# Performance work log

Hardware: AMD Instinct MI355X
Metric: run time of the kernel (lower is better)

## Reference

```python
import jax, jax.numpy as jnp
import numpy as np

NUM_WIRES = 20
DEPTH = 4


def setup_inputs() -> dict:
    key = jax.random.key(0)
    x = jax.random.normal(key, (NUM_WIRES,), dtype=jnp.float32)
    return {"x": x}


def _apply_1q(state, gate, wire):
    # state: flat [2^n] complex; apply 2x2 gate on `wire`
    s = state.reshape(2 ** wire, 2, -1)
    return jnp.einsum('ab,ibj->iaj', gate, s).reshape(-1)


def _apply_cnot(state, control):
    # CNOT on adjacent wires (control, control+1): flip target where control==1
    s = state.reshape(2 ** control, 2, 2, -1)
    s = jnp.concatenate([s[:, :1], s[:, 1:, ::-1]], axis=1)
    return s.reshape(-1)


def _simulate(x):
    n = NUM_WIRES
    state = jnp.zeros(2 ** n, dtype=jnp.complex64).at[0].set(1.0)
    half = (x.astype(jnp.float32) * 0.5)
    c = jnp.cos(half).astype(jnp.complex64)  # [n]
    s = jnp.sin(half).astype(jnp.complex64)  # [n]
    for _ in range(DEPTH):
        for w in range(n):
            cw, sw = c[w], s[w]
            rx = jnp.stack([jnp.stack([cw, -1j * sw]), jnp.stack([-1j * sw, cw])])
            ry = jnp.stack([jnp.stack([cw, -sw]), jnp.stack([sw, cw])])
            state = _apply_1q(state, rx, w)
            state = _apply_1q(state, ry, w)
        for w in range(n - 1):
            state = _apply_cnot(state, w)
    probs = jnp.abs(state) ** 2  # real float32 [2^n]
    expz = []
    for i in range(n):
        p = probs.reshape(2 ** i, 2, -1).sum(axis=(0, 2))
        expz.append(p[0] - p[1])
    return jnp.stack(expz).astype(jnp.float32)  # [n] <Z_i>


def reference(x):
    return _simulate(x)
```

## Files before the change

### kernel.cpp

```cpp
#include <hip/hip_runtime.h>


#define NW 20

__device__ __forceinline__ float2 cmul(float2 a, float2 b) {
    return make_float2(a.x*b.x - a.y*b.y, a.x*b.y + a.y*b.x);
}

__device__ __forceinline__ void apply_gate(float2& a0, float2& a1,
                                           float2 u00, float2 u01,
                                           float2 u10, float2 u11) {
    float2 b0, b1;
    b0.x = u00.x*a0.x - u00.y*a0.y + u01.x*a1.x - u01.y*a1.y;
    b0.y = u00.x*a0.y + u00.y*a0.x + u01.x*a1.y + u01.y*a1.x;
    b1.x = u10.x*a0.x - u10.y*a0.y + u11.x*a1.x - u11.y*a1.y;
    b1.y = u10.x*a0.y + u10.y*a0.x + u11.x*a1.y + u11.y*a1.x;
    a0 = b0; a1 = b1;
}

__device__ __forceinline__ unsigned swz(unsigned l) { return l ^ ((l >> 3) & 14u); }

__global__ void prep_gates(const float* __restrict__ x, float2* __restrict__ G) {
    int w = threadIdx.x;
    if (w < NW) {
        float h = 0.5f * x[w];
        float c = cosf(h), s = sinf(h);
        float cc = c*c, ss = s*s, cs = c*s;
        G[w*4+0] = make_float2(cc,  ss);
        G[w*4+1] = make_float2(-cs, -cs);
        G[w*4+2] = make_float2(cs,  -cs);
        G[w*4+3] = make_float2(cc,  -ss);
    }
}

template<int MODE>
__global__ __launch_bounds__(1024) void stageA(const float2* __restrict__ src,
                                               float2* __restrict__ dst,
                                               const float2* __restrict__ G) {
    __shared__ float4 ldsv[2048];
    float2* lds = (float2*)ldsv;
    unsigned t   = threadIdx.x;
    unsigned H   = blockIdx.x;
    unsigned Hp  = H ^ (H >> 1);
    unsigned inj = (H & 1u) << 11;
    unsigned l   = t * 4u;
    unsigned gl  = (l ^ (l >> 1)) ^ inj;

    float2 a0, a1, a2, a3;
    if (MODE == 1) {
        const float4* qp = (const float4*)(src + ((size_t)Hp << 12) + (gl & ~3u));
        float4 q0 = qp[0], q1 = qp[1];
        float2 e0 = make_float2(q0.x, q0.y), e1 = make_float2(q0.z, q0.w);
        float2 e2 = make_float2(q1.x, q1.y), e3 = make_float2(q1.z, q1.w);
        bool s1 = (gl & 1u) != 0u, s2 = (gl & 2u) != 0u;
        float2 f0 = s1 ? e1 : e0, f1 = s1 ? e0 : e1;
        float2 f2 = s1 ? e3 : e2, f3 = s1 ? e2 : e3;
        float2 g0 = s2 ? f2 : f0, g1 = s2 ? f3 : f1;
        float2 g2 = s2 ? f0 : f2, g3 = s2 ? f1 : f3;
        a0 = g0; a1 = g1; a2 = g3; a3 = g2;
    } else {
        float2 P = make_float2(1.0f, 0.0f);
        #pragma unroll
        for (int b = 12; b <= 19; b++)
            P = cmul(P, G[(19-b)*4 + (int)((Hp >> (b-12)) & 1u)*2]);
        #pragma unroll
        for (int b = 2; b <= 11; b++)
            P = cmul(P, G[(19-b)*4 + (int)((gl >> b) & 1u)*2]);
        float2 aa[4];
        #pragma unroll
        for (int k = 0; k < 4; k++) {
            unsigned mm = (gl ^ (unsigned)(k ^ (k >> 1))) & 3u;
            float2 f = cmul(G[19*4 + (int)(mm & 1u)*2], G[18*4 + (int)((mm >> 1) & 1u)*2]);
            aa[k] = cmul(P, f);
        }
        a0 = aa[0]; a1 = aa[1]; a2 = aa[2]; a3 = aa[3];
    }

    {
        float2 u00 = G[76], u01 = G[77], u10 = G[78], u11 = G[79];
        apply_gate(a0, a1, u00, u01, u10, u11);
        apply_gate(a2, a3, u00, u01, u10, u11);
    }
    {
        float2 u00 = G[72], u01 = G[73], u10 = G[74], u11 = G[75];
        apply_gate(a0, a2, u00, u01, u10, u11);
        apply_gate(a1, a3, u00, u01, u10, u11);
    }
    lds[swz(l+0u)] = a0; lds[swz(l+1u)] = a1;
    lds[swz(l+2u)] = a2; lds[swz(l+3u)] = a3;
    __syncthreads();

    #pragma unroll
    for (int p = 2; p <= 11; p++) {
        int w = 19 - p;
        float2 u00 = G[w*4], u01 = G[w*4+1], u10 = G[w*4+2], u11 = G[w*4+3];
        unsigned mask = (1u << p) - 1u;
        #pragma unroll
        for (int i = 0; i < 2; i++) {
            unsigned kk = (unsigned)i*1024u + t;
            unsigned l0 = ((kk & ~mask) << 1) | (kk & mask);
            unsigned l1 = l0 | (1u << p);
            unsigned s0 = swz(l0), s1i = swz(l1);
            float2 b0 = lds[s0], b1 = lds[s1i];
            apply_gate(b0, b1, u00, u01, u10, u11);
            if (p < 11) { lds[s0] = b0; lds[s1i] = b1; }
            else {
                dst[((size_t)H << 12) + l0] = b0;
                dst[((size_t)H << 12) + l1] = b1;
            }
        }
        if (p < 11) __syncthreads();
    }
}

template<int FUSE>
__global__ __launch_bounds__(1024) void stageB(float2* __restrict__ st,
                                               const float2* __restrict__ G,
                                               float* __restrict__ partial) {
    __shared__ float4 ldsv[2048];
    float2* lds = (float2*)ldsv;
    unsigned t  = threadIdx.x;
    unsigned bb = blockIdx.x;
    unsigned m  = t & 15u, hk = t >> 4;
    unsigned h0 = hk << 1;
    unsigned hsA = h0, hsB = h0 | 1u, hsC = h0 | 128u, hsD = h0 | 129u;
    size_t base = ((size_t)bb << 4) | m;
    float2 a0 = st[((size_t)hsA << 12) | base];
    float2 a1 = st[((size_t)hsB << 12) | base];
    float2 a2 = st[((size_t)hsC << 12) | base];
    float2 a3 = st[((size_t)hsD << 12) | base];

    {
        float2 u00 = G[28], u01 = G[29], u10 = G[30], u11 = G[31];
        apply_gate(a0, a1, u00, u01, u10, u11);
        apply_gate(a2, a3, u00, u01, u10, u11);
    }
    {
        float2 u00 = G[0], u01 = G[1], u10 = G[2], u11 = G[3];
        apply_gate(a0, a2, u00, u01, u10, u11);
        apply_gate(a1, a3, u00, u01, u10, u11);
    }
    lds[(hsA << 4) | m] = a0; lds[(hsB << 4) | m] = a1;
    lds[(hsC << 4) | m] = a2; lds[(hsD << 4) | m] = a3;
    __syncthreads();

    #pragma unroll
    for (int q = 1; q <= 5; q++) {
        int w = 7 - q;
        float2 u00 = G[w*4], u01 = G[w*4+1], u10 = G[w*4+2], u11 = G[w*4+3];
        unsigned mq = (1u << q) - 1u;
        #pragma unroll
        for (int i = 0; i < 2; i++) {
            unsigned kk = (unsigned)i*1024u + t;
            unsigned mm = kk & 15u, hh = kk >> 4;
            unsigned hA = ((hh & ~mq) << 1) | (hh & mq);
            unsigned ci0 = (hA << 4) | mm, ci1 = ci0 | (1u << (4 + q));
            float2 b0 = lds[ci0], b1 = lds[ci1];
            apply_gate(b0, b1, u00, u01, u10, u11);
            lds[ci0] = b0; lds[ci1] = b1;
        }
        __syncthreads();
    }

    float acc[NW];
    if (FUSE) {
        #pragma unroll
        for (int w = 0; w < NW; w++) acc[w] = 0.0f;
    }
    {
        float2 u00 = G[4], u01 = G[5], u10 = G[6], u11 = G[7];
        #pragma unroll
        for (int i = 0; i < 2; i++) {
            unsigned kk = (unsigned)i*1024u + t;
            unsigned mm = kk & 15u, hh = kk >> 4;
            unsigned hA = ((hh & ~63u) << 1) | (hh & 63u);
            unsigned ci0 = (hA << 4) | mm, ci1 = ci0 | (1u << 10);
            float2 b0 = lds[ci0], b1 = lds[ci1];
            apply_gate(b0, b1, u00, u01, u10, u11);
            if (!FUSE) {
                st[((size_t)(ci0 >> 4) << 12) | ((size_t)bb << 4) | mm] = b0;
                st[((size_t)(ci1 >> 4) << 12) | ((size_t)bb << 4) | mm] = b1;
            } else {
                #pragma unroll
                for (int e = 0; e < 2; e++) {
                    unsigned ci = e ? ci1 : ci0;
                    float2 bv  = e ? b1 : b0;
                    unsigned Y = ((ci >> 4) << 12) | (bb << 4) | mm;
                    unsigned y = Y;
                    y ^= y >> 1; y ^= y >> 2; y ^= y >> 4; y ^= y >> 8; y ^= y >> 16;
                    float p = bv.x*bv.x + bv.y*bv.y;
                    #pragma unroll
                    for (int w = 0; w < NW; w++) {
                        unsigned bit = (y >> (19 - w)) & 1u;
                        acc[w] += __uint_as_float(__float_as_uint(p) | (bit << 31));
                    }
                }
            }
        }
    }

    if (FUSE) {
        __syncthreads();
        float* redf = (float*)ldsv;
        #pragma unroll
        for (int w = 0; w < NW; w++) {
            float v = acc[w];
            #pragma unroll
            for (int off = 32; off; off >>= 1) v += __shfl_down(v, off, 64);
            if ((t & 63u) == 0u) redf[(t >> 6)*NW + w] = v;
        }
        __syncthreads();
        if (t < NW) {
            float s = 0.0f;
            #pragma unroll
            for (int wv = 0; wv < 16; wv++) s += redf[wv*NW + (int)t];
            partial[bb*NW + t] = s;
        }
    }
}

__global__ __launch_bounds__(256) void reduce_out(const float* __restrict__ partial,
                                                  float* __restrict__ out) {
    __shared__ float red[4*NW];
    unsigned t = threadIdx.x;
    float vals[NW];
    #pragma unroll
    for (int w = 0; w < NW; w++) vals[w] = partial[t*NW + w];
    #pragma unroll
    for (int w = 0; w < NW; w++) {
        float v = vals[w];
        #pragma unroll
        for (int off = 32; off; off >>= 1) v += __shfl_down(v, off, 64);
        if ((t & 63u) == 0u) red[(t >> 6)*NW + w] = v;
    }
    __syncthreads();
    if (t < NW) out[t] = red[t] + red[NW+t] + red[2*NW+t] + red[3*NW+t];
}

extern "C" void kernel_launch(void* const* d_in, const int* in_sizes, int n_in,
                              void* d_out, int out_size, void* d_ws, size_t ws_size,
                              hipStream_t stream) {
    (void)in_sizes; (void)n_in; (void)out_size; (void)ws_size;
    const float* x = (const float*)d_in[0];
    float* out = (float*)d_out;

    char* ws = (char*)d_ws;
    float2* gates   = (float2*)ws;
    float*  partial = (float*)(ws + 1024);
    float2* buf0    = (float2*)(ws + 65536);
    float2* buf1    = (float2*)(ws + 65536 + (size_t)(8u << 20));

    prep_gates<<<1, 32, 0, stream>>>(x, gates);
    stageA<0><<<256, 1024, 0, stream>>>(buf1 , buf0, gates);
    stageB<0><<<256, 1024, 0, stream>>>(buf0, gates, nullptr);
    stageA<1><<<256, 1024, 0, stream>>>(buf0, buf1, gates);
    stageB<0><<<256, 1024, 0, stream>>>(buf1, gates, nullptr);
    stageA<1><<<256, 1024, 0, stream>>>(buf1, buf0, gates);
    stageB<1><<<256, 1024, 0, stream>>>(buf0, gates, partial);
    reduce_out<<<1, 256, 0, stream>>>(partial, out);
}
```

Measured before the change: 77.15 us.

## Keep eight amplitudes per thread and apply gates via registers and lane shuffles

Both stage kernels now hold eight amplitudes per thread in registers. Gates on register bits are applied directly, bit positions are exchanged across lanes with xor-shuffles, and only a single shared-memory transpose with one barrier remains, instead of ten barriered LDS passes. Blocks shrink to 512 threads. The fused final stage also derives most Z expectations from a single parity-signed difference instead of accumulating per element. This trades LDS traffic and synchronisation for more register pressure and shuffle instructions.

Measured after the change: 72.75 us. -5.7%, faster.

```diff
diff --git a/kernel.cpp b/kernel.cpp
--- a/kernel.cpp
+++ b/kernel.cpp
@@ -18,7 +18,36 @@
     a0 = b0; a1 = b1;
 }
 
-__device__ __forceinline__ unsigned swz(unsigned l) { return l ^ ((l >> 3) & 14u); }
+__device__ __forceinline__ float2 shflx(float2 v, int m) {
+    float2 r;
+    r.x = __shfl_xor(v.x, m, 64);
+    r.y = __shfl_xor(v.y, m, 64);
+    return r;
+}
+
+template<int A>
+__device__ __forceinline__ void gate_regbit(float2 (&amp)[8], const float2* __restrict__ Gw) {
+    float2 u00 = Gw[0], u01 = Gw[1], u10 = Gw[2], u11 = Gw[3];
+    #pragma unroll
+    for (int r = 0; r < 8; r++)
+        if (!(r & (1 << A)))
+            apply_gate(amp[r], amp[r | (1 << A)], u00, u01, u10, u11);
+}
+
+template<int A, int LM>
+__device__ __forceinline__ void swap_reg_lane(float2 (&amp)[8], unsigned lane) {
+    bool hb = (lane & (unsigned)LM) != 0u;
+    #pragma unroll
+    for (int r = 0; r < 8; r++) {
+        if (!(r & (1 << A))) {
+            float2 lo = amp[r], hi = amp[r | (1 << A)];
+            float2 xs = hb ? lo : hi;
+            float2 ys = shflx(xs, LM);
+            amp[r]            = hb ? ys : lo;
+            amp[r | (1 << A)] = hb ? hi : ys;
+        }
+    }
+}
 
 __global__ void prep_gates(const float* __restrict__ x, float2* __restrict__ G) {
     int w = threadIdx.x;
@@ -34,186 +63,155 @@
 }
 
 template<int MODE>
-__global__ __launch_bounds__(1024) void stageA(const float2* __restrict__ src,
-                                               float2* __restrict__ dst,
-                                               const float2* __restrict__ G) {
-    __shared__ float4 ldsv[2048];
-    float2* lds = (float2*)ldsv;
-    unsigned t   = threadIdx.x;
-    unsigned H   = blockIdx.x;
-    unsigned Hp  = H ^ (H >> 1);
-    unsigned inj = (H & 1u) << 11;
-    unsigned l   = t * 4u;
-    unsigned gl  = (l ^ (l >> 1)) ^ inj;
-
-    float2 a0, a1, a2, a3;
+__global__ __launch_bounds__(512) void stageA(const float2* __restrict__ src,
+                                              float2* __restrict__ dst,
+                                              const float2* __restrict__ G) {
+    __shared__ float2 lds[4096];
+    const unsigned t = threadIdx.x;
+    const unsigned lane = t & 63u, wv = t >> 6;
+    const unsigned H   = blockIdx.x;
+    const unsigned Hp  = H ^ (H >> 1);
+    const unsigned inj = (H & 1u) << 11;
+    const unsigned lb  = (wv << 9) | (lane << 3);
+    const unsigned gb  = (lb ^ (lb >> 1)) ^ inj;
+
+    float2 amp[8];
     if (MODE == 1) {
-        const float4* qp = (const float4*)(src + ((size_t)Hp << 12) + (gl & ~3u));
-        float4 q0 = qp[0], q1 = qp[1];
-        float2 e0 = make_float2(q0.x, q0.y), e1 = make_float2(q0.z, q0.w);
-        float2 e2 = make_float2(q1.x, q1.y), e3 = make_float2(q1.z, q1.w);
-        bool s1 = (gl & 1u) != 0u, s2 = (gl & 2u) != 0u;
-        float2 f0 = s1 ? e1 : e0, f1 = s1 ? e0 : e1;
-        float2 f2 = s1 ? e3 : e2, f3 = s1 ? e2 : e3;
-        float2 g0 = s2 ? f2 : f0, g1 = s2 ? f3 : f1;
-        float2 g2 = s2 ? f0 : f2, g3 = s2 ? f1 : f3;
-        a0 = g0; a1 = g1; a2 = g3; a3 = g2;
+        const float4* q = (const float4*)(src + ((size_t)Hp << 12) + (gb & ~7u));
+        float4 q0 = q[0], q1 = q[1], q2 = q[2], q3 = q[3];
+        float2 e0 = make_float2(q0.x,q0.y), e1 = make_float2(q0.z,q0.w);
+        float2 e2 = make_float2(q1.x,q1.y), e3 = make_float2(q1.z,q1.w);
+        float2 e4 = make_float2(q2.x,q2.y), e5 = make_float2(q2.z,q2.w);
+        float2 e6 = make_float2(q3.x,q3.y), e7 = make_float2(q3.z,q3.w);
+        bool f = (gb & 4u) != 0u;
+        amp[0] = f ? e4 : e0;  amp[1] = f ? e5 : e1;
+        amp[2] = f ? e7 : e3;  amp[3] = f ? e6 : e2;
+        amp[4] = f ? e2 : e6;  amp[5] = f ? e3 : e7;
+        amp[6] = f ? e1 : e5;  amp[7] = f ? e0 : e4;
     } else {
         float2 P = make_float2(1.0f, 0.0f);
         #pragma unroll
         for (int b = 12; b <= 19; b++)
             P = cmul(P, G[(19-b)*4 + (int)((Hp >> (b-12)) & 1u)*2]);
         #pragma unroll
-        for (int b = 2; b <= 11; b++)
-            P = cmul(P, G[(19-b)*4 + (int)((gl >> b) & 1u)*2]);
-        float2 aa[4];
-        #pragma unroll
-        for (int k = 0; k < 4; k++) {
-            unsigned mm = (gl ^ (unsigned)(k ^ (k >> 1))) & 3u;
-            float2 f = cmul(G[19*4 + (int)(mm & 1u)*2], G[18*4 + (int)((mm >> 1) & 1u)*2]);
-            aa[k] = cmul(P, f);
-        }
-        a0 = aa[0]; a1 = aa[1]; a2 = aa[2]; a3 = aa[3];
-    }
-
-    {
-        float2 u00 = G[76], u01 = G[77], u10 = G[78], u11 = G[79];
-        apply_gate(a0, a1, u00, u01, u10, u11);
-        apply_gate(a2, a3, u00, u01, u10, u11);
-    }
-    {
-        float2 u00 = G[72], u01 = G[73], u10 = G[74], u11 = G[75];
-        apply_gate(a0, a2, u00, u01, u10, u11);
-        apply_gate(a1, a3, u00, u01, u10, u11);
-    }
-    lds[swz(l+0u)] = a0; lds[swz(l+1u)] = a1;
-    lds[swz(l+2u)] = a2; lds[swz(l+3u)] = a3;
+        for (int b = 3; b <= 11; b++)
+            P = cmul(P, G[(19-b)*4 + (int)((gb >> b) & 1u)*2]);
+        float2 Tt[8];
+        #pragma unroll
+        for (int j = 0; j < 8; j++) {
+            float2 v = cmul(G[18*4 + ((j>>1)&1)*2], G[19*4 + (j&1)*2]);
+            v = cmul(G[17*4 + ((j>>2)&1)*2], v);
+            Tt[j] = cmul(P, v);
+        }
+        bool f = (gb & 4u) != 0u;
+        amp[0] = f ? Tt[4] : Tt[0];  amp[1] = f ? Tt[5] : Tt[1];
+        amp[2] = f ? Tt[7] : Tt[3];  amp[3] = f ? Tt[6] : Tt[2];
+        amp[4] = f ? Tt[2] : Tt[6];  amp[5] = f ? Tt[3] : Tt[7];
+        amp[6] = f ? Tt[1] : Tt[5];  amp[7] = f ? Tt[0] : Tt[4];
+    }
+
+    gate_regbit<0>(amp, G + 19*4);
+    gate_regbit<1>(amp, G + 18*4);
+    gate_regbit<2>(amp, G + 17*4);
+    swap_reg_lane<0,1>(amp, lane);
+    swap_reg_lane<1,2>(amp, lane);
+    swap_reg_lane<2,4>(amp, lane);
+    gate_regbit<0>(amp, G + 16*4);
+    gate_regbit<1>(amp, G + 15*4);
+    gate_regbit<2>(amp, G + 14*4);
+    swap_reg_lane<0,8>(amp, lane);
+    swap_reg_lane<1,16>(amp, lane);
+    swap_reg_lane<2,32>(amp, lane);
+    gate_regbit<0>(amp, G + 13*4);
+    gate_regbit<1>(amp, G + 12*4);
+    gate_regbit<2>(amp, G + 11*4);
+    #pragma unroll
+    for (int k = 0; k < 8; k++) lds[(wv << 9) | ((unsigned)k << 6) | lane] = amp[k];
     __syncthreads();
-
-    #pragma unroll
-    for (int p = 2; p <= 11; p++) {
-        int w = 19 - p;
-        float2 u00 = G[w*4], u01 = G[w*4+1], u10 = G[w*4+2], u11 = G[w*4+3];
-        unsigned mask = (1u << p) - 1u;
-        #pragma unroll
-        for (int i = 0; i < 2; i++) {
-            unsigned kk = (unsigned)i*1024u + t;
-            unsigned l0 = ((kk & ~mask) << 1) | (kk & mask);
-            unsigned l1 = l0 | (1u << p);
-            unsigned s0 = swz(l0), s1i = swz(l1);
-            float2 b0 = lds[s0], b1 = lds[s1i];
-            apply_gate(b0, b1, u00, u01, u10, u11);
-            if (p < 11) { lds[s0] = b0; lds[s1i] = b1; }
-            else {
-                dst[((size_t)H << 12) + l0] = b0;
-                dst[((size_t)H << 12) + l1] = b1;
-            }
-        }
-        if (p < 11) __syncthreads();
-    }
+    #pragma unroll
+    for (int k = 0; k < 8; k++) amp[k] = lds[((unsigned)k << 9) | (wv << 6) | lane];
+    gate_regbit<0>(amp, G + 10*4);
+    gate_regbit<1>(amp, G +  9*4);
+    gate_regbit<2>(amp, G +  8*4);
+    float2* d = dst + ((size_t)H << 12);
+    #pragma unroll
+    for (int k = 0; k < 8; k++) d[((unsigned)k << 9) | (wv << 6) | lane] = amp[k];
 }
 
 template<int FUSE>
-__global__ __launch_bounds__(1024) void stageB(float2* __restrict__ st,
-                                               const float2* __restrict__ G,
-                                               float* __restrict__ partial) {
-    __shared__ float4 ldsv[2048];
-    float2* lds = (float2*)ldsv;
-    unsigned t  = threadIdx.x;
-    unsigned bb = blockIdx.x;
-    unsigned m  = t & 15u, hk = t >> 4;
-    unsigned h0 = hk << 1;
-    unsigned hsA = h0, hsB = h0 | 1u, hsC = h0 | 128u, hsD = h0 | 129u;
-    size_t base = ((size_t)bb << 4) | m;
-    float2 a0 = st[((size_t)hsA << 12) | base];
-    float2 a1 = st[((size_t)hsB << 12) | base];
-    float2 a2 = st[((size_t)hsC << 12) | base];
-    float2 a3 = st[((size_t)hsD << 12) | base];
-
-    {
-        float2 u00 = G[28], u01 = G[29], u10 = G[30], u11 = G[31];
-        apply_gate(a0, a1, u00, u01, u10, u11);
-        apply_gate(a2, a3, u00, u01, u10, u11);
-    }
-    {
-        float2 u00 = G[0], u01 = G[1], u10 = G[2], u11 = G[3];
-        apply_gate(a0, a2, u00, u01, u10, u11);
-        apply_gate(a1, a3, u00, u01, u10, u11);
-    }
-    lds[(hsA << 4) | m] = a0; lds[(hsB << 4) | m] = a1;
-    lds[(hsC << 4) | m] = a2; lds[(hsD << 4) | m] = a3;
+__global__ __launch_bounds__(512) void stageB(float2* __restrict__ st,
+                                              const float2* __restrict__ G,
+                                              float* __restrict__ partial) {
+    __shared__ float2 lds[4096];
+    const unsigned t = threadIdx.x, lane = t & 63u, wv = t >> 6;
+    const unsigned bb = blockIdx.x;
+    const unsigned m = lane & 15u, l45 = lane >> 4;
+
+    float2 amp[8];
+    #pragma unroll
+    for (int k = 0; k < 8; k++) {
+        unsigned h = (unsigned)k | (l45 << 3) | (wv << 5);
+        amp[k] = st[((size_t)h << 12) | (bb << 4) | m];
+    }
+    gate_regbit<0>(amp, G + 7*4);
+    gate_regbit<1>(amp, G + 6*4);
+    gate_regbit<2>(amp, G + 5*4);
+    swap_reg_lane<0,16>(amp, lane);
+    swap_reg_lane<1,32>(amp, lane);
+    gate_regbit<0>(amp, G + 4*4);
+    gate_regbit<1>(amp, G + 3*4);
+    #pragma unroll
+    for (int k = 0; k < 8; k++) {
+        unsigned li = lane | ((((unsigned)k >> 2) & 1u) << 6) | (((unsigned)k & 1u) << 7)
+                    | ((((unsigned)k >> 1) & 1u) << 8) | (wv << 9);
+        lds[li] = amp[k];
+    }
     __syncthreads();
-
-    #pragma unroll
-    for (int q = 1; q <= 5; q++) {
-        int w = 7 - q;
-        float2 u00 = G[w*4], u01 = G[w*4+1], u10 = G[w*4+2], u11 = G[w*4+3];
-        unsigned mq = (1u << q) - 1u;
-        #pragma unroll
-        for (int i = 0; i < 2; i++) {
-            unsigned kk = (unsigned)i*1024u + t;
-            unsigned mm = kk & 15u, hh = kk >> 4;
-            unsigned hA = ((hh & ~mq) << 1) | (hh & mq);
-            unsigned ci0 = (hA << 4) | mm, ci1 = ci0 | (1u << (4 + q));
-            float2 b0 = lds[ci0], b1 = lds[ci1];
-            apply_gate(b0, b1, u00, u01, u10, u11);
-            lds[ci0] = b0; lds[ci1] = b1;
-        }
+    #pragma unroll
+    for (int k = 0; k < 8; k++) amp[k] = lds[lane | (wv << 6) | ((unsigned)k << 9)];
+    gate_regbit<0>(amp, G + 2*4);
+    gate_regbit<1>(amp, G + 1*4);
+    gate_regbit<2>(amp, G + 0*4);
+
+    if (!FUSE) {
+        #pragma unroll
+        for (int k = 0; k < 8; k++) {
+            unsigned h = l45 | (wv << 2) | ((unsigned)k << 5);
+            st[((size_t)h << 12) | (bb << 4) | m] = amp[k];
+        }
+    } else {
+        float p[8];
+        #pragma unroll
+        for (int k = 0; k < 8; k++) p[k] = amp[k].x*amp[k].x + amp[k].y*amp[k].y;
+        float Se = p[0]+p[3]+p[5]+p[6];
+        float So = p[1]+p[2]+p[4]+p[7];
+        float D  = Se - So;
+        float S0 = (p[0]+p[1]+p[2]+p[3]) - (p[4]+p[5]+p[6]+p[7]);
+        float S1 = (p[0]+p[1]+p[6]+p[7]) - (p[2]+p[3]+p[4]+p[5]);
+        unsigned hlow = l45 | (wv << 2);
+        unsigned v = (hlow << 12) | (bb << 4) | m;
+        unsigned cm = v; cm ^= cm >> 1; cm ^= cm >> 2; cm ^= cm >> 4;
+        cm ^= cm >> 8; cm ^= cm >> 16;
+        float acc[NW];
+        acc[0] = S0; acc[1] = S1; acc[2] = D;
+        #pragma unroll
+        for (int w = 3; w < NW; w++)
+            acc[w] = ((cm >> (19 - w)) & 1u) ? -D : D;
+
         __syncthreads();
-    }
-
-    float acc[NW];
-    if (FUSE) {
-        #pragma unroll
-        for (int w = 0; w < NW; w++) acc[w] = 0.0f;
-    }
-    {
-        float2 u00 = G[4], u01 = G[5], u10 = G[6], u11 = G[7];
-        #pragma unroll
-        for (int i = 0; i < 2; i++) {
-            unsigned kk = (unsigned)i*1024u + t;
-            unsigned mm = kk & 15u, hh = kk >> 4;
-            unsigned hA = ((hh & ~63u) << 1) | (hh & 63u);
-            unsigned ci0 = (hA << 4) | mm, ci1 = ci0 | (1u << 10);
-            float2 b0 = lds[ci0], b1 = lds[ci1];
-            apply_gate(b0, b1, u00, u01, u10, u11);
-            if (!FUSE) {
-                st[((size_t)(ci0 >> 4) << 12) | ((size_t)bb << 4) | mm] = b0;
-                st[((size_t)(ci1 >> 4) << 12) | ((size_t)bb << 4) | mm] = b1;
-            } else {
-                #pragma unroll
-                for (int e = 0; e < 2; e++) {
-                    unsigned ci = e ? ci1 : ci0;
-                    float2 bv  = e ? b1 : b0;
-                    unsigned Y = ((ci >> 4) << 12) | (bb << 4) | mm;
-                    unsigned y = Y;
-                    y ^= y >> 1; y ^= y >> 2; y ^= y >> 4; y ^= y >> 8; y ^= y >> 16;
-                    float p = bv.x*bv.x + bv.y*bv.y;
-                    #pragma unroll
-                    for (int w = 0; w < NW; w++) {
-                        unsigned bit = (y >> (19 - w)) & 1u;
-                        acc[w] += __uint_as_float(__float_as_uint(p) | (bit << 31));
-                    }
-                }
-            }
-        }
-    }
-
-    if (FUSE) {
-        __syncthreads();
-        float* redf = (float*)ldsv;
+        float* red = (float*)lds;
         #pragma unroll
         for (int w = 0; w < NW; w++) {
-            float v = acc[w];
+            float s = acc[w];
             #pragma unroll
-            for (int off = 32; off; off >>= 1) v += __shfl_down(v, off, 64);
-            if ((t & 63u) == 0u) redf[(t >> 6)*NW + w] = v;
+            for (int off = 32; off; off >>= 1) s += __shfl_down(s, off, 64);
+            if (lane == 0) red[wv*NW + w] = s;
         }
         __syncthreads();
         if (t < NW) {
             float s = 0.0f;
             #pragma unroll
-            for (int wv = 0; wv < 16; wv++) s += redf[wv*NW + (int)t];
+            for (int w8 = 0; w8 < 8; w8++) s += red[w8*NW + (int)t];
             partial[bb*NW + t] = s;
         }
     }
@@ -251,11 +249,11 @@
     float2* buf1    = (float2*)(ws + 65536 + (size_t)(8u << 20));
 
     prep_gates<<<1, 32, 0, stream>>>(x, gates);
-    stageA<0><<<256, 1024, 0, stream>>>(buf1 , buf0, gates);
-    stageB<0><<<256, 1024, 0, stream>>>(buf0, gates, nullptr);
-    stageA<1><<<256, 1024, 0, stream>>>(buf0, buf1, gates);
-    stageB<0><<<256, 1024, 0, stream>>>(buf1, gates, nullptr);
-    stageA<1><<<256, 1024, 0, stream>>>(buf1, buf0, gates);
-    stageB<1><<<256, 1024, 0, stream>>>(buf0, gates, partial);
+    stageA<0><<<256, 512, 0, stream>>>(buf1 , buf0, gates);
+    stageB<0><<<256, 512, 0, stream>>>(buf0, gates, nullptr);
+    stageA<1><<<256, 512, 0, stream>>>(buf0, buf1, gates);
+    stageB<0><<<256, 512, 0, stream>>>(buf1, gates, nullptr);
+    stageA<1><<<256, 512, 0, stream>>>(buf1, buf0, gates);
+    stageB<1><<<256, 512, 0, stream>>>(buf0, gates, partial);
     reduce_out<<<1, 256, 0, stream>>>(partial, out);
 }
```
